# Kernel tuning notes

Measured on AMD Instinct MI355X. Metric: run time of the kernel, lower is better.

Reference implementation:

```python
import jax, jax.numpy as jnp
import numpy as np

B, N, U = 8, 2048, 256
BN_EPS = 1e-3  # keras BatchNormalization default epsilon
ADJ_DENSITY = 0.008  # ~16 neighbors per node on average


def setup_inputs() -> dict:
    key = jax.random.key(0)
    ks = jax.random.split(key, 16)
    s = 0.05  # weight scale ('random_normal' init is small-stddev in keras)
    x = jax.random.normal(ks[0], (B, N, U), jnp.float32)
    # sparse binary adjacency stored dense (per-sample SpMM pattern)
    adj = (jax.random.uniform(ks[1], (B, N, N)) < ADJ_DENSITY).astype(jnp.float32)
    nodal_mask = jnp.ones((B, N), jnp.float32)
    return {
        'x': x, 'adj': adj, 'nodal_mask': nodal_mask,
        'W_lin': jax.random.normal(ks[2], (U, U)) * s, 'b_lin': jnp.zeros((U,)),
        'Wq_mp': jax.random.normal(ks[3], (3, U, U)) * s, 'bq_mp': jnp.zeros((3, U)),
        'Wk_mp': jax.random.normal(ks[4], (3, U, U)) * s, 'bk_mp': jnp.zeros((3, U)),
        'Wv_mp': jax.random.normal(ks[5], (3, U, U)) * s, 'bv_mp': jnp.zeros((3, U)),
        'Wk_att': jax.random.normal(ks[6], (U, U)) * s,
        'Wv_att': jax.random.normal(ks[7], (U, U)) * s,
        'Wq_att': jax.random.normal(ks[8], (U, U)) * s,
        'Wo_att': jax.random.normal(ks[9], (U, U)) * s,
        'bn_gamma': jnp.ones((U,)), 'bn_beta': jnp.zeros((U,)),
        'bn_mean': jnp.zeros((U,)), 'bn_var': jnp.ones((U,)),
        'W_proj': jax.random.normal(ks[10], (U, U)) * s, 'b_proj': jnp.zeros((U,)),
        'W_res': jax.random.normal(ks[11], (U, U)) * s, 'b_res': jnp.zeros((U,)),
    }


def _dympn(x, adj, Ws, bs, mask):
    # 3 message-passing layers, each applied K_l=2 times (inference value)
    for i in range(3):
        for _ in range(2):
            xn = jnp.einsum('bmn,bnd->bmd', adj, x)  # batched SpMM (graph_conv mode)
            x = jax.nn.silu(jnp.einsum('bmd,de->bme', xn, Ws[i]) + bs[i])
    return x * mask[:, :, None]


def reference(x, adj, nodal_mask, W_lin, b_lin, Wq_mp, bq_mp, Wk_mp, bk_mp,
              Wv_mp, bv_mp, Wk_att, Wv_att, Wq_att, Wo_att,
              bn_gamma, bn_beta, bn_mean, bn_var, W_proj, b_proj, W_res, b_res):
    initial_x = x
    adj = jax.lax.stop_gradient(adj)
    h = jnp.einsum('bnd,de->bne', x, W_lin) + b_lin
    q = _dympn(h, adj, Wq_mp, bq_mp, nodal_mask)
    k = _dympn(h, adj, Wk_mp, bk_mp, nodal_mask)
    v = _dympn(h, adj, Wv_mp, bv_mp, nodal_mask)
    # linear attention
    m = nodal_mask[:, :, None]
    pk = jax.nn.silu(jnp.einsum('bnd,de->bne', k, Wk_att) * m)
    pv = jnp.einsum('bnd,de->bne', v, Wv_att) * m
    pq = jnp.einsum('bnd,de->bne', q, Wq_att)
    kv = jnp.einsum('bnd,bne->bde', pk, pv)       # [B,U,U]
    attn = jnp.einsum('bnd,bde->bne', pq, kv)
    attn = jnp.einsum('bnd,de->bne', attn, Wo_att)
    # batch norm (inference: moving stats) over last axis
    y = attn + initial_x
    y = bn_gamma * (y - bn_mean) * jax.lax.rsqrt(bn_var + BN_EPS) + bn_beta
    out = jax.nn.silu(jnp.einsum('bnd,de->bne', y, W_proj) + b_proj)
    out = out + jnp.einsum('bnd,de->bne', initial_x, W_res) + b_res
    out = out * nodal_mask[:, :, None]
    return out
```

## Files before the change

### kernel.cpp

```cpp
#include <hip/hip_runtime.h>
#include <stdint.h>

#define NB 8
#define NN 2048
#define NU 256
#define CAP 64
#define BNEPS 0.001f

typedef __attribute__((ext_vector_type(8))) short short8;
typedef __attribute__((ext_vector_type(4))) float floatx4;
typedef unsigned short u16;
typedef unsigned int u32;

__device__ __forceinline__ float bf2f(u16 u) {
  union { u32 i; float f; } c; c.i = ((u32)u) << 16; return c.f;
}
__device__ __forceinline__ u16 f2bf(float f) {
  union { float f; u32 i; } c; c.f = f;
  return (u16)((c.i + 0x7fffu + ((c.i >> 16) & 1u)) >> 16);
}
__device__ __forceinline__ void splitbf(float a, u16& h, u16& l) {
  h = f2bf(a);
  l = f2bf(a - bf2f(h));
}

enum : unsigned {
  F_BIAS = 2u, F_SILU = 4u, F_MASKPRE = 8u, F_MASKPOST = 16u,
  F_ADDX = 32u, F_BN = 64u, F_ADDT = 128u, F_BPERMAT = 512u,
  F_TPLANES = 1024u, F_OUTHL = 2048u
};

#define TP_MAT 524288
#define TP_LO  4194304
#define MSZ ((size_t)NN * NU)

struct WPtrs { const float* p[16]; };

__global__ __launch_bounds__(256) void prologue_k(
    WPtrs wp, u16* __restrict__ wdst,
    const float* __restrict__ x, u16* __restrict__ xdst, size_t xLo,
    const float* __restrict__ adj, int* __restrict__ cnt, int* __restrict__ idx)
{
  int bid = blockIdx.x;
  int tid = threadIdx.x;
  __shared__ int c0;
  if (bid < 512) {
    int gid = bid * 256 + tid;
    int mat = gid >> 13;
    int rem = gid & 8191;
    int kb = rem >> 10;
    int n = (rem >> 2) & 255;
    int slot = rem & 3;
    int qv = (slot - (n >> 1)) & 3;
    int k0 = kb * 32 + qv * 8;
    const float* W = wp.p[mat];
    u32 oh[4], ol[4];
#pragma unroll
    for (int t2 = 0; t2 < 4; t2++) {
      float f0 = W[(size_t)(k0 + 2 * t2) * 256 + n];
      float f1 = W[(size_t)(k0 + 2 * t2 + 1) * 256 + n];
      u16 h0, l0, h1, l1;
      splitbf(f0, h0, l0);
      splitbf(f1, h1, l1);
      oh[t2] = (u32)h0 | ((u32)h1 << 16);
      ol[t2] = (u32)l0 | ((u32)l1 << 16);
    }
    uint4 qh; qh.x = oh[0]; qh.y = oh[1]; qh.z = oh[2]; qh.w = oh[3];
    uint4 ql; ql.x = ol[0]; ql.y = ol[1]; ql.z = ol[2]; ql.w = ol[3];
    *(uint4*)(wdst + (size_t)gid * 8) = qh;
    *(uint4*)(wdst + 1048576 + (size_t)gid * 8) = ql;
  } else if (bid < 4608) {
    size_t i = ((size_t)(bid - 512) * 256 + tid) * 4;
    float4 v = *(const float4*)(x + i);
    u16 h0, l0, h1, l1, h2, l2, h3, l3;
    splitbf(v.x, h0, l0); splitbf(v.y, h1, l1);
    splitbf(v.z, h2, l2); splitbf(v.w, h3, l3);
    uint2 H; H.x = (u32)h0 | ((u32)h1 << 16); H.y = (u32)h2 | ((u32)h3 << 16);
    uint2 L; L.x = (u32)l0 | ((u32)l1 << 16); L.y = (u32)l2 | ((u32)l3 << 16);
    *(uint2*)(xdst + i) = H;
    *(uint2*)(xdst + xLo + i) = L;
  } else {
    int row = bid - 4608;
    const float* base = adj + (size_t)row * NN;
    if (tid == 0) c0 = 0;
    __syncthreads();
#pragma unroll
    for (int j = 0; j < 8; j++) {
      int n = j * 256 + tid;
      if (base[n] != 0.f) {
        int p = atomicAdd(&c0, 1);
        if (p < CAP) idx[(size_t)row * CAP + p] = n;
      }
    }
    __syncthreads();
    if (tid == 0) cnt[row] = (c0 < CAP ? c0 : CAP);
  }
}

template <unsigned F>
__device__ __forceinline__ void gemm_epi(
    floatx4 (&acc)[2][2], int b, int bm, int w, int m16, int q,
    const float* __restrict__ bias, const float* __restrict__ mask,
    const float* __restrict__ xf32,
    const float* __restrict__ gma, const float* __restrict__ bta,
    const float* __restrict__ bmu, const float* __restrict__ bvr,
    const float* __restrict__ addt, void* __restrict__ outp, size_t oLo)
{
#pragma unroll
  for (int mt = 0; mt < 2; mt++) {
    if (F & F_TPLANES) {
      u16* oh = (u16*)outp + (size_t)b * TP_MAT;
      u16* ol = oh + TP_LO;
      int gr0 = bm + mt * 16 + q * 4;
#pragma unroll
      for (int nt = 0; nt < 2; nt++) {
        int col = w * 32 + nt * 16 + m16;
        u16 hh[4], ll[4];
#pragma unroll
        for (int r = 0; r < 4; r++) {
          float t2 = acc[mt][nt][r];
          float mv = mask[b * NN + gr0 + r];
          if (F & F_MASKPRE) t2 *= mv;
          if (F & F_SILU) t2 = t2 / (1.f + __expf(-t2));
          if (F & F_MASKPOST) t2 *= mv;
          splitbf(t2, hh[r], ll[r]);
        }
        uint2 H2, L2v;
        H2.x = (u32)hh[0] | ((u32)hh[1] << 16);
        H2.y = (u32)hh[2] | ((u32)hh[3] << 16);
        L2v.x = (u32)ll[0] | ((u32)ll[1] << 16);
        L2v.y = (u32)ll[2] | ((u32)ll[3] << 16);
        *(uint2*)(oh + (size_t)col * 2048 + gr0) = H2;
        *(uint2*)(ol + (size_t)col * 2048 + gr0) = L2v;
      }
    } else {
#pragma unroll
      for (int r = 0; r < 4; r++) {
        int gr = bm + mt * 16 + q * 4 + r;
        float mval = 1.f;
        if (F & (F_MASKPRE | F_MASKPOST)) mval = mask[b * NN + gr];
#pragma unroll
        for (int nt = 0; nt < 2; nt++) {
          int col = w * 32 + nt * 16 + m16;
          float t2 = acc[mt][nt][r];
          if (F & F_BIAS) t2 += bias[col];
          if (F & F_MASKPRE) t2 *= mval;
          if (F & F_SILU) t2 = t2 / (1.f + __expf(-t2));
          if (F & F_ADDX) t2 += xf32[((size_t)b * NN + gr) * NU + col];
          if (F & F_BN) t2 = gma[col] * (t2 - bmu[col]) * rsqrtf(bvr[col] + BNEPS) + bta[col];
          if (F & F_ADDT) t2 += addt[((size_t)b * NN + gr) * NU + col];
          if (F & F_MASKPOST) t2 *= mval;
          size_t o = ((size_t)b * NN + gr) * NU + col;
          if (F & F_OUTHL) {
            u16 h0, l0;
            splitbf(t2, h0, l0);
            ((u16*)outp)[o] = h0;
            ((u16*)outp)[o + oLo] = l0;
          } else {
            ((float*)outp)[o] = t2;
          }
        }
      }
    }
  }
}

template <int NG, unsigned SF, unsigned F0, unsigned F1, unsigned F2, bool DK = false>
__global__ __launch_bounds__(512, 8) void gemm_k(
    const u16* __restrict__ A0, const u16* __restrict__ A1, const u16* __restrict__ A2,
    size_t aLo,
    const u16* __restrict__ W0, const u16* __restrict__ W1, const u16* __restrict__ W2,
    size_t wLo,
    const float* __restrict__ b0, const float* __restrict__ b1, const float* __restrict__ b2,
    const float* __restrict__ mask,
    const float* __restrict__ xf32,
    const float* __restrict__ gma, const float* __restrict__ bta,
    const float* __restrict__ bmu, const float* __restrict__ bvr,
    const float* __restrict__ addt,
    void* __restrict__ o0, void* __restrict__ o1, void* __restrict__ o2,
    size_t oLo,
    const float* __restrict__ gsrc,
    const float* __restrict__ sb0, const float* __restrict__ sb1, const float* __restrict__ sb2,
    const int* __restrict__ ncnt, const int* __restrict__ nidx)
{
  const int tid = threadIdx.x;
  const int id = blockIdx.x;
  const int xcd = id & 7;
  const int t = id >> 3;
  const int chain = (NG == 1) ? 0 : (t >> 6);
  const int xt = (NG == 1) ? t : (t & 63);
  const int b = xcd;
  const int bm = xt * 32;

  __shared__ alignas(16) u16 Ah[32 * 264];
  __shared__ alignas(16) u16 Al[32 * 264];

  const u16* Wsel = (chain == 0) ? W0 : (chain == 1 ? W1 : W2);
  if (F0 & F_BPERMAT) Wsel = W0 + (size_t)b * 65536;
  const u16* Whi = Wsel;
  const u16* Wlo = Whi + wLo;

  const int lane = tid & 63;
  const int w = tid >> 6;

  if constexpr (SF != 0u) {
    const float* __restrict__ gm = gsrc + ((size_t)chain * 8 + b) * MSZ;
    const float* sb = (chain == 0) ? sb0 : (chain == 1 ? sb1 : sb2);
    const int c = lane * 4;
    float4 bb = *(const float4*)(sb + c);
    const int r0 = w * 4;
    int cnts[4];
    const int* ips[4];
    float4 av[4];
    int rowids[4];
#pragma unroll
    for (int i = 0; i < 4; i++) {
      rowids[i] = b * NN + bm + r0 + i;
      cnts[i] = ncnt[rowids[i]];
      ips[i] = nidx + (size_t)rowids[i] * CAP;
      av[i].x = av[i].y = av[i].z = av[i].w = 0.f;
    }
    int maxc = cnts[0];
    maxc = cnts[1] > maxc ? cnts[1] : maxc;
    maxc = cnts[2] > maxc ? cnts[2] : maxc;
    maxc = cnts[3] > maxc ? cnts[3] : maxc;
    for (int e = 0; e + 4 <= maxc; e += 4) {
#pragma unroll
      for (int i = 0; i < 4; i++) {
        if (e + 4 <= cnts[i]) {
          int4 i4 = *(const int4*)(ips[i] + e);
          float4 v0 = *(const float4*)(gm + ((size_t)i4.x << 8) + c);
          float4 v1 = *(const float4*)(gm + ((size_t)i4.y << 8) + c);
          float4 v2 = *(const float4*)(gm + ((size_t)i4.z << 8) + c);
          float4 v3 = *(const float4*)(gm + ((size_t)i4.w << 8) + c);
          av[i].x += v0.x + v1.x + v2.x + v3.x;
          av[i].y += v0.y + v1.y + v2.y + v3.y;
          av[i].z += v0.z + v1.z + v2.z + v3.z;
          av[i].w += v0.w + v1.w + v2.w + v3.w;
        }
      }
    }
#pragma unroll
    for (int i = 0; i < 4; i++) {
      for (int e = cnts[i] & ~3; e < cnts[i]; e++) {
        float4 v = *(const float4*)(gm + ((size_t)ips[i][e] << 8) + c);
        av[i].x += v.x; av[i].y += v.y; av[i].z += v.z; av[i].w += v.w;
      }
    }
#pragma unroll
    for (int i = 0; i < 4; i++) {
      float ov[4] = {av[i].x + bb.x, av[i].y + bb.y, av[i].z + bb.z, av[i].w + bb.w};
      float mv = (SF & F_MASKPOST) ? mask[rowids[i]] : 1.f;
      u16 hh[4], ll[4];
#pragma unroll
      for (int j = 0; j < 4; j++) {
        float t2 = ov[j];
        if (SF & F_SILU) t2 = t2 / (1.f + __expf(-t2));
        if (SF & F_MASKPOST) t2 *= mv;
        splitbf(t2, hh[j], ll[j]);
      }
      uint2 H; H.x = (u32)hh[0] | ((u32)hh[1] << 16); H.y = (u32)hh[2] | ((u32)hh[3] << 16);
      uint2 L; L.x = (u32)ll[0] | ((u32)ll[1] << 16); L.y = (u32)ll[2] | ((u32)ll[3] << 16);
      *(uint2*)&Ah[(r0 + i) * 264 + c] = H;
      *(uint2*)&Al[(r0 + i) * 264 + c] = L;
    }
  } else {
    const u16* Abase = (chain == 0) ? A0 : (chain == 1 ? A1 : A2);
    const u16* Ahp = Abase + (size_t)b * MSZ;
    const u16* Alp = Ahp + aLo;
    {
      int s = tid;
      int r = s >> 4;
      int c = (s & 15) << 4;
      size_t ao = (size_t)(bm + r) * 256 + c;
      *(uint4*)&Ah[r * 264 + c] = *(const uint4*)(Ahp + ao);
      *(uint4*)&Ah[r * 264 + c + 8] = *(const uint4*)(Ahp + ao + 8);
      *(uint4*)&Al[r * 264 + c] = *(const uint4*)(Alp + ao);
      *(uint4*)&Al[r * 264 + c + 8] = *(const uint4*)(Alp + ao + 8);
    }
  }
  __syncthreads();

  const int m16 = lane & 15;
  const int q = lane >> 4;

  floatx4 acc[2][2];
#pragma unroll
  for (int i = 0; i < 2; i++)
#pragma unroll
    for (int j = 0; j < 2; j++) acc[i][j] = (floatx4){0.f, 0.f, 0.f, 0.f};

#pragma unroll
  for (int kk = 0; kk < 8; kk++) {
    short8 bh[2], bl2[2];
#pragma unroll
    for (int nt = 0; nt < 2; nt++) {
      int n = w * 32 + nt * 16 + m16;
      size_t off = (size_t)kk * 8192 + (size_t)n * 32 + (size_t)(((q + (n >> 1)) & 3) * 8);
      bh[nt] = *(const short8*)(Whi + off);
      bl2[nt] = *(const short8*)(Wlo + off);
    }
#pragma unroll
    for (int mt = 0; mt < 2; mt++) {
      int row = mt * 16 + m16;
      short8 ah = *(const short8*)&Ah[row * 264 + kk * 32 + q * 8];
      short8 al2 = *(const short8*)&Al[row * 264 + kk * 32 + q * 8];
#pragma unroll
      for (int nt = 0; nt < 2; nt++) {
        acc[mt][nt] = __builtin_amdgcn_mfma_f32_16x16x32_bf16(ah, bh[nt], acc[mt][nt], 0, 0, 0);
        acc[mt][nt] = __builtin_amdgcn_mfma_f32_16x16x32_bf16(al2, bh[nt], acc[mt][nt], 0, 0, 0);
        acc[mt][nt] = __builtin_amdgcn_mfma_f32_16x16x32_bf16(ah, bl2[nt], acc[mt][nt], 0, 0, 0);
      }
    }
  }

  if constexpr (DK) {
#pragma unroll
    for (int mt = 0; mt < 2; mt++)
#pragma unroll
      for (int nt = 0; nt < 2; nt++) {
        int col = w * 32 + nt * 16 + m16;
        float bp = b1[col];
#pragma unroll
        for (int r = 0; r < 4; r++) {
          float t2 = acc[mt][nt][r] + bp;
          acc[mt][nt][r] = t2 / (1.f + __expf(-t2));
        }
      }
    __syncthreads();
    {
      const u16* Ahp = A1 + (size_t)b * MSZ;
      const u16* Alp = Ahp + aLo;
      int s = tid;
      int r = s >> 4;
      int c = (s & 15) << 4;
      size_t ao = (size_t)(bm + r) * 256 + c;
      *(uint4*)&Ah[r * 264 + c] = *(const uint4*)(Ahp + ao);
      *(uint4*)&Ah[r * 264 + c + 8] = *(const uint4*)(Ahp + ao + 8);
      *(uint4*)&Al[r * 264 + c] = *(const uint4*)(Alp + ao);
      *(uint4*)&Al[r * 264 + c + 8] = *(const uint4*)(Alp + ao + 8);
    }
    __syncthreads();
    const u16* W1h = W1;
    const u16* W1l = W1 + wLo;
#pragma unroll
    for (int kk = 0; kk < 8; kk++) {
      short8 bh[2], bl2[2];
#pragma unroll
      for (int nt = 0; nt < 2; nt++) {
        int n = w * 32 + nt * 16 + m16;
        size_t off = (size_t)kk * 8192 + (size_t)n * 32 + (size_t)(((q + (n >> 1)) & 3) * 8);
        bh[nt] = *(const short8*)(W1h + off);
        bl2[nt] = *(const short8*)(W1l + off);
      }
#pragma unroll
      for (int mt = 0; mt < 2; mt++) {
        int row = mt * 16 + m16;
        short8 ah = *(const short8*)&Ah[row * 264 + kk * 32 + q * 8];
        short8 al2 = *(const short8*)&Al[row * 264 + kk * 32 + q * 8];
#pragma unroll
        for (int nt = 0; nt < 2; nt++) {
          acc[mt][nt] = __builtin_amdgcn_mfma_f32_16x16x32_bf16(ah, bh[nt], acc[mt][nt], 0, 0, 0);
          acc[mt][nt] = __builtin_amdgcn_mfma_f32_16x16x32_bf16(al2, bh[nt], acc[mt][nt], 0, 0, 0);
          acc[mt][nt] = __builtin_amdgcn_mfma_f32_16x16x32_bf16(ah, bl2[nt], acc[mt][nt], 0, 0, 0);
        }
      }
    }
  }

  if (NG == 1 || chain == 0)
    gemm_epi<F0>(acc, b, bm, w, m16, q, b0, mask, xf32, gma, bta, bmu, bvr, addt, o0, oLo);
  else if (chain == 1)
    gemm_epi<F1>(acc, b, bm, w, m16, q, b1, mask, xf32, gma, bta, bmu, bvr, addt, o1, oLo);
  else
    gemm_epi<F2>(acc, b, bm, w, m16, q, b2, mask, xf32, gma, bta, bmu, bvr, addt, o2, oLo);
}

__global__ __launch_bounds__(256, 2) void kv_k(
    const u16* __restrict__ pkT, const u16* __restrict__ pvT, float* __restrict__ part)
{
  int et = blockIdx.x * 128;
  int dt = blockIdx.y * 128;
  int z = blockIdx.z;
  int b = z & 7;
  int p = z >> 3;
  int tid = threadIdx.x;
  int lane = tid & 63, w = tid >> 6;
  int m16 = lane & 15, q = lane >> 4;

  const u16* pkh = pkT + (size_t)b * TP_MAT;
  const u16* pkl = pkh + TP_LO;
  const u16* pvh = pvT + (size_t)b * TP_MAT;
  const u16* pvl = pvh + TP_LO;

  int d_base = dt + (w >> 1) * 64 + m16;
  int e_base = et + (w & 1) * 64 + m16;

  floatx4 acc[4][4];
#pragma unroll
  for (int i = 0; i < 4; i++)
#pragma unroll
    for (int j = 0; j < 4; j++) acc[i][j] = (floatx4){0.f, 0.f, 0.f, 0.f};

#pragma unroll
  for (int kt = 0; kt < 8; kt++) {
    int kc = p * 256 + kt * 32 + q * 8;
    short8 ah[4], al[4], bh[4], bl[4];
#pragma unroll
    for (int mt = 0; mt < 4; mt++) {
      size_t o = (size_t)(d_base + mt * 16) * 2048 + kc;
      ah[mt] = *(const short8*)(pkh + o);
      al[mt] = *(const short8*)(pkl + o);
    }
#pragma unroll
    for (int nt = 0; nt < 4; nt++) {
      size_t o = (size_t)(e_base + nt * 16) * 2048 + kc;
      bh[nt] = *(const short8*)(pvh + o);
      bl[nt] = *(const short8*)(pvl + o);
    }
#pragma unroll
    for (int mt = 0; mt < 4; mt++)
#pragma unroll
      for (int nt = 0; nt < 4; nt++) {
        acc[mt][nt] = __builtin_amdgcn_mfma_f32_16x16x32_bf16(ah[mt], bh[nt], acc[mt][nt], 0, 0, 0);
        acc[mt][nt] = __builtin_amdgcn_mfma_f32_16x16x32_bf16(al[mt], bh[nt], acc[mt][nt], 0, 0, 0);
        acc[mt][nt] = __builtin_amdgcn_mfma_f32_16x16x32_bf16(ah[mt], bl[nt], acc[mt][nt], 0, 0, 0);
      }
  }

#pragma unroll
  for (int mt = 0; mt < 4; mt++)
#pragma unroll
    for (int r = 0; r < 4; r++) {
      int d = dt + (w >> 1) * 64 + mt * 16 + q * 4 + r;
#pragma unroll
      for (int nt = 0; nt < 4; nt++) {
        int e = et + (w & 1) * 64 + nt * 16 + m16;
        part[(size_t)z * 65536 + (size_t)d * 256 + e] = acc[mt][nt][r];
      }
    }
}

__global__ __launch_bounds__(256) void kv_conv_k(const float* __restrict__ part, u16* __restrict__ dst)
{
  int gid = blockIdx.x * 256 + threadIdx.x;
  int b = gid >> 13;
  int rem = gid & 8191;
  int kb = rem >> 10;
  int e = (rem >> 2) & 255;
  int slot = rem & 3;
  int qv = (slot - (e >> 1)) & 3;
  int d0 = kb * 32 + qv * 8;
  const float* src = part + (size_t)b * 65536 + (size_t)d0 * 256 + e;
  u32 oh[4], ol[4];
#pragma unroll
  for (int t2 = 0; t2 < 4; t2++) {
    float s0 = 0.f, s1 = 0.f;
#pragma unroll
    for (int pp = 0; pp < 8; pp++) {
      const float* sp = src + (size_t)pp * 524288 + t2 * 512;
      s0 += sp[0];
      s1 += sp[256];
    }
    u16 h0, l0, h1, l1;
    splitbf(s0, h0, l0);
    splitbf(s1, h1, l1);
    oh[t2] = (u32)h0 | ((u32)h1 << 16);
    ol[t2] = (u32)l0 | ((u32)l1 << 16);
  }
  uint4 qh; qh.x = oh[0]; qh.y = oh[1]; qh.z = oh[2]; qh.w = oh[3];
  uint4 ql; ql.x = ol[0]; ql.y = ol[1]; ql.z = ol[2]; ql.w = ol[3];
  *(uint4*)(dst + (size_t)gid * 8) = qh;
  *(uint4*)(dst + 524288 + (size_t)gid * 8) = ql;
}

extern "C" void kernel_launch(void* const* d_in, const int* in_sizes, int n_in,
                              void* d_out, int out_size, void* d_ws, size_t ws_size,
                              hipStream_t stream)
{
  const float* x = (const float*)d_in[0];
  const float* adj = (const float*)d_in[1];
  const float* mask = (const float*)d_in[2];
  const float* W_lin = (const float*)d_in[3];
  const float* b_lin = (const float*)d_in[4];
  const float* Wq_mp = (const float*)d_in[5];
  const float* bq_mp = (const float*)d_in[6];
  const float* Wk_mp = (const float*)d_in[7];
  const float* bk_mp = (const float*)d_in[8];
  const float* Wv_mp = (const float*)d_in[9];
  const float* bv_mp = (const float*)d_in[10];
  const float* Wk_att = (const float*)d_in[11];
  const float* Wv_att = (const float*)d_in[12];
  const float* Wq_att = (const float*)d_in[13];
  const float* Wo_att = (const float*)d_in[14];
  const float* bn_gamma = (const float*)d_in[15];
  const float* bn_beta = (const float*)d_in[16];
  const float* bn_mean = (const float*)d_in[17];
  const float* bn_var = (const float*)d_in[18];
  const float* W_proj = (const float*)d_in[19];
  const float* b_proj = (const float*)d_in[20];
  const float* W_res = (const float*)d_in[21];
  const float* b_res = (const float*)d_in[22];

  char* ws = (char*)d_ws;
  int* CNT    = (int*)(ws + 0);
  int* IDX    = (int*)(ws + (1ull << 20));
  u16* WSZ    = (u16*)(ws + (5ull << 20));
  u16* KVS    = (u16*)(ws + (9ull << 20));
  float* KVP  = (float*)(ws + (11ull << 20));
  u16* XHL    = (u16*)(ws + (27ull << 20));
  u16* HHL    = (u16*)(ws + (43ull << 20));
  float* GA   = (float*)(ws + (59ull << 20));
  float* GB   = (float*)(ws + (107ull << 20));
  u16* PKT    = (u16*)(ws + (155ull << 20));
  u16* PVT    = (u16*)(ws + (171ull << 20));
  u16* ATT    = (u16*)(ws + (187ull << 20));
  u16* YHL    = (u16*)(ws + (203ull << 20));

  const size_t WLO = 1048576;
  const size_t KLO = 524288;
  const size_t A8  = 8 * MSZ;

  u16* PQHL = HHL;

  WPtrs wp;
  wp.p[0] = W_lin;
  wp.p[1] = Wq_mp; wp.p[2] = Wq_mp + 65536; wp.p[3] = Wq_mp + 131072;
  wp.p[4] = Wk_mp; wp.p[5] = Wk_mp + 65536; wp.p[6] = Wk_mp + 131072;
  wp.p[7] = Wv_mp; wp.p[8] = Wv_mp + 65536; wp.p[9] = Wv_mp + 131072;
  wp.p[10] = Wk_att; wp.p[11] = Wv_att; wp.p[12] = Wq_att; wp.p[13] = Wo_att;
  wp.p[14] = W_proj; wp.p[15] = W_res;
  prologue_k<<<20992, 256, 0, stream>>>(wp, WSZ, x, XHL, A8, adj, CNT, IDX);

  gemm_k<1, 0u, F_BIAS | F_OUTHL, 0u, 0u><<<512, 512, 0, stream>>>(
      XHL, XHL, XHL, A8, WSZ, WSZ, WSZ, WLO,
      b_lin, nullptr, nullptr, mask, nullptr,
      bn_gamma, bn_beta, bn_mean, bn_var, nullptr,
      HHL, nullptr, nullptr, A8,
      nullptr, nullptr, nullptr, nullptr, CNT, IDX);

  gemm_k<3, 0u, 0u, 0u, 0u><<<1536, 512, 0, stream>>>(
      HHL, HHL, HHL, A8,
      WSZ + (size_t)1 * 65536, WSZ + (size_t)4 * 65536, WSZ + (size_t)7 * 65536, WLO,
      nullptr, nullptr, nullptr, mask, nullptr,
      bn_gamma, bn_beta, bn_mean, bn_var, nullptr,
      GA, GA + 8 * MSZ, GA + 16 * MSZ, 0,
      nullptr, nullptr, nullptr, nullptr, CNT, IDX);

  for (int s = 1; s < 6; s++) {
    int iw = s >> 1;
    int ib = (s - 1) >> 1;
    float* Gin = (s & 1) ? GA : GB;
    float* Gout = (s & 1) ? GB : GA;
    gemm_k<3, F_BIAS | F_SILU, 0u, 0u, 0u><<<1536, 512, 0, stream>>>(
        nullptr, nullptr, nullptr, 0,
        WSZ + (size_t)(1 + iw) * 65536, WSZ + (size_t)(4 + iw) * 65536,
        WSZ + (size_t)(7 + iw) * 65536, WLO,
        nullptr, nullptr, nullptr, mask, nullptr,
        bn_gamma, bn_beta, bn_mean, bn_var, nullptr,
        Gout, Gout + 8 * MSZ, Gout + 16 * MSZ, 0,
        Gin, bq_mp + ib * 256, bk_mp + ib * 256, bv_mp + ib * 256, CNT, IDX);
  }

  gemm_k<3, F_BIAS | F_SILU | F_MASKPOST,
         F_OUTHL, F_SILU | F_MASKPRE | F_TPLANES, F_MASKPOST | F_TPLANES>
      <<<1536, 512, 0, stream>>>(
      nullptr, nullptr, nullptr, 0,
      WSZ + (size_t)12 * 65536, WSZ + (size_t)10 * 65536, WSZ + (size_t)11 * 65536, WLO,
      nullptr, nullptr, nullptr, mask, nullptr,
      bn_gamma, bn_beta, bn_mean, bn_var, nullptr,
      PQHL, PKT, PVT, A8,
      GB, bq_mp + 512, bk_mp + 512, bv_mp + 512, CNT, IDX);

  kv_k<<<dim3(2, 2, 64), 256, 0, stream>>>(PKT, PVT, KVP);
  kv_conv_k<<<256, 256, 0, stream>>>(KVP, KVS);

  gemm_k<1, 0u, F_BPERMAT | F_OUTHL, 0u, 0u><<<512, 512, 0, stream>>>(
      PQHL, PQHL, PQHL, A8, KVS, KVS, KVS, KLO,
      nullptr, nullptr, nullptr, mask, nullptr,
      bn_gamma, bn_beta, bn_mean, bn_var, nullptr,
      ATT, nullptr, nullptr, A8,
      nullptr, nullptr, nullptr, nullptr, CNT, IDX);

  gemm_k<1, 0u, F_ADDX | F_BN | F_OUTHL, 0u, 0u><<<512, 512, 0, stream>>>(
      ATT, ATT, ATT, A8,
      WSZ + (size_t)13 * 65536, nullptr, nullptr, WLO,
      nullptr, nullptr, nullptr, mask, x,
      bn_gamma, bn_beta, bn_mean, bn_var, nullptr,
      YHL, nullptr, nullptr, A8,
      nullptr, nullptr, nullptr, nullptr, CNT, IDX);

  gemm_k<1, 0u, F_BIAS | F_MASKPOST, 0u, 0u, true><<<512, 512, 0, stream>>>(
      YHL, XHL, YHL, A8,
      WSZ + (size_t)14 * 65536, WSZ + (size_t)15 * 65536, nullptr, WLO,
      b_res, b_proj, nullptr, mask, nullptr,
      bn_gamma, bn_beta, bn_mean, bn_var, nullptr,
      d_out, nullptr, nullptr, 0,
      nullptr, nullptr, nullptr, nullptr, CNT, IDX);

  (void)in_sizes; (void)n_in; (void)out_size; (void)ws_size;
}
```

Before: 759.3 us.

## Pad SpMM gathers with zero row, branchless neighbor loop, nontemporal stores

Pads each neighbor index list to a multiple of four with -1 entries. Each per-batch G buffer gets a zeroed 256-float guard row in front, so index -1 reads zeros. This makes the SpMM gather loop branchless, with no remainder loop. Nontemporal stores are also added for the GEMM epilogue outputs and the kv partials, to reduce cache pollution from streaming writes. The costs are a changed workspace layout, extra prologue blocks to zero the guard rows, and some wasted gathers on padded entries.

```diff
diff --git a/kernel.cpp b/kernel.cpp
--- a/kernel.cpp
+++ b/kernel.cpp
@@ -6,11 +6,13 @@
 #define NU 256
 #define CAP 64
 #define BNEPS 0.001f
+#define GSTR ((size_t)(NN * NU + 256))
 
 typedef __attribute__((ext_vector_type(8))) short short8;
 typedef __attribute__((ext_vector_type(4))) float floatx4;
 typedef unsigned short u16;
 typedef unsigned int u32;
+typedef unsigned long long u64;
 
 __device__ __forceinline__ float bf2f(u16 u) {
   union { u32 i; float f; } c; c.i = ((u32)u) << 16; return c.f;
@@ -27,7 +29,7 @@
 enum : unsigned {
   F_BIAS = 2u, F_SILU = 4u, F_MASKPRE = 8u, F_MASKPOST = 16u,
   F_ADDX = 32u, F_BN = 64u, F_ADDT = 128u, F_BPERMAT = 512u,
-  F_TPLANES = 1024u, F_OUTHL = 2048u
+  F_TPLANES = 1024u, F_OUTHL = 2048u, F_NTOUT = 4096u, F_GSTRIDE = 8192u
 };
 
 #define TP_MAT 524288
@@ -39,7 +41,8 @@
 __global__ __launch_bounds__(256) void prologue_k(
     WPtrs wp, u16* __restrict__ wdst,
     const float* __restrict__ x, u16* __restrict__ xdst, size_t xLo,
-    const float* __restrict__ adj, int* __restrict__ cnt, int* __restrict__ idx)
+    const float* __restrict__ adj, int* __restrict__ cnt, int* __restrict__ idx,
+    float* __restrict__ ga, float* __restrict__ gb)
 {
   int bid = blockIdx.x;
   int tid = threadIdx.x;
@@ -79,7 +82,7 @@
     uint2 L; L.x = (u32)l0 | ((u32)l1 << 16); L.y = (u32)l2 | ((u32)l3 << 16);
     *(uint2*)(xdst + i) = H;
     *(uint2*)(xdst + xLo + i) = L;
-  } else {
+  } else if (bid < 20992) {
     int row = bid - 4608;
     const float* base = adj + (size_t)row * NN;
     if (tid == 0) c0 = 0;
@@ -93,7 +96,13 @@
       }
     }
     __syncthreads();
-    if (tid == 0) cnt[row] = (c0 < CAP ? c0 : CAP);
+    int cc = (c0 < CAP ? c0 : CAP);
+    for (int p = cc + tid; p < CAP; p += 256) idx[(size_t)row * CAP + p] = -1;
+    if (tid == 0) cnt[row] = cc;
+  } else {
+    int g = bid - 20992;
+    float* base = (g < 24 ? ga : gb) + (size_t)(g % 24) * GSTR;
+    base[tid] = 0.f;
   }
 }
 
@@ -130,8 +139,13 @@
         H2.y = (u32)hh[2] | ((u32)hh[3] << 16);
         L2v.x = (u32)ll[0] | ((u32)ll[1] << 16);
         L2v.y = (u32)ll[2] | ((u32)ll[3] << 16);
-        *(uint2*)(oh + (size_t)col * 2048 + gr0) = H2;
-        *(uint2*)(ol + (size_t)col * 2048 + gr0) = L2v;
+        if (F & F_NTOUT) {
+          __builtin_nontemporal_store(*(u64*)&H2, (u64*)(oh + (size_t)col * 2048 + gr0));
+          __builtin_nontemporal_store(*(u64*)&L2v, (u64*)(ol + (size_t)col * 2048 + gr0));
+        } else {
+          *(uint2*)(oh + (size_t)col * 2048 + gr0) = H2;
+          *(uint2*)(ol + (size_t)col * 2048 + gr0) = L2v;
+        }
       }
     } else {
 #pragma unroll
@@ -150,14 +164,22 @@
           if (F & F_BN) t2 = gma[col] * (t2 - bmu[col]) * rsqrtf(bvr[col] + BNEPS) + bta[col];
           if (F & F_ADDT) t2 += addt[((size_t)b * NN + gr) * NU + col];
           if (F & F_MASKPOST) t2 *= mval;
-          size_t o = ((size_t)b * NN + gr) * NU + col;
+          size_t o;
+          if (F & F_GSTRIDE) o = (size_t)b * GSTR + (size_t)gr * NU + col;
+          else o = ((size_t)b * NN + gr) * NU + col;
           if (F & F_OUTHL) {
             u16 h0, l0;
             splitbf(t2, h0, l0);
-            ((u16*)outp)[o] = h0;
-            ((u16*)outp)[o + oLo] = l0;
+            if (F & F_NTOUT) {
+              __builtin_nontemporal_store(h0, (u16*)outp + o);
+              __builtin_nontemporal_store(l0, (u16*)outp + o + oLo);
+            } else {
+              ((u16*)outp)[o] = h0;
+              ((u16*)outp)[o + oLo] = l0;
+            }
           } else {
-            ((float*)outp)[o] = t2;
+            if (F & F_NTOUT) __builtin_nontemporal_store(t2, (float*)outp + o);
+            else ((float*)outp)[o] = t2;
           }
         }
       }
@@ -204,47 +226,37 @@
   const int w = tid >> 6;
 
   if constexpr (SF != 0u) {
-    const float* __restrict__ gm = gsrc + ((size_t)chain * 8 + b) * MSZ;
+    const float* __restrict__ gm = gsrc + (size_t)(chain * 8 + b) * GSTR + 256;
     const float* sb = (chain == 0) ? sb0 : (chain == 1 ? sb1 : sb2);
     const int c = lane * 4;
     float4 bb = *(const float4*)(sb + c);
     const int r0 = w * 4;
-    int cnts[4];
     const int* ips[4];
     float4 av[4];
     int rowids[4];
+    int maxc = 0;
 #pragma unroll
     for (int i = 0; i < 4; i++) {
       rowids[i] = b * NN + bm + r0 + i;
-      cnts[i] = ncnt[rowids[i]];
+      int cn = ncnt[rowids[i]];
+      maxc = cn > maxc ? cn : maxc;
       ips[i] = nidx + (size_t)rowids[i] * CAP;
       av[i].x = av[i].y = av[i].z = av[i].w = 0.f;
     }
-    int maxc = cnts[0];
-    maxc = cnts[1] > maxc ? cnts[1] : maxc;
-    maxc = cnts[2] > maxc ? cnts[2] : maxc;
-    maxc = cnts[3] > maxc ? cnts[3] : maxc;
-    for (int e = 0; e + 4 <= maxc; e += 4) {
+    maxc = (maxc + 3) & ~3;
+#pragma unroll 1
+    for (int e = 0; e < maxc; e += 4) {
 #pragma unroll
       for (int i = 0; i < 4; i++) {
-        if (e + 4 <= cnts[i]) {
-          int4 i4 = *(const int4*)(ips[i] + e);
-          float4 v0 = *(const float4*)(gm + ((size_t)i4.x << 8) + c);
-          float4 v1 = *(const float4*)(gm + ((size_t)i4.y << 8) + c);
-          float4 v2 = *(const float4*)(gm + ((size_t)i4.z << 8) + c);
-          float4 v3 = *(const float4*)(gm + ((size_t)i4.w << 8) + c);
-          av[i].x += v0.x + v1.x + v2.x + v3.x;
-          av[i].y += v0.y + v1.y + v2.y + v3.y;
-          av[i].z += v0.z + v1.z + v2.z + v3.z;
-          av[i].w += v0.w + v1.w + v2.w + v3.w;
-        }
-      }
-    }
-#pragma unroll
-    for (int i = 0; i < 4; i++) {
-      for (int e = cnts[i] & ~3; e < cnts[i]; e++) {
-        float4 v = *(const float4*)(gm + ((size_t)ips[i][e] << 8) + c);
-        av[i].x += v.x; av[i].y += v.y; av[i].z += v.z; av[i].w += v.w;
+        int4 i4 = *(const int4*)(ips[i] + e);
+        float4 v0 = *(const float4*)(gm + (ptrdiff_t)i4.x * 256 + c);
+        float4 v1 = *(const float4*)(gm + (ptrdiff_t)i4.y * 256 + c);
+        float4 v2 = *(const float4*)(gm + (ptrdiff_t)i4.z * 256 + c);
+        float4 v3 = *(const float4*)(gm + (ptrdiff_t)i4.w * 256 + c);
+        av[i].x += v0.x + v1.x + v2.x + v3.x;
+        av[i].y += v0.y + v1.y + v2.y + v3.y;
+        av[i].z += v0.z + v1.z + v2.z + v3.z;
+        av[i].w += v0.w + v1.w + v2.w + v3.w;
       }
     }
 #pragma unroll
@@ -436,7 +448,8 @@
 #pragma unroll
       for (int nt = 0; nt < 4; nt++) {
         int e = et + (w & 1) * 64 + nt * 16 + m16;
-        part[(size_t)z * 65536 + (size_t)d * 256 + e] = acc[mt][nt][r];
+        __builtin_nontemporal_store(acc[mt][nt][r],
+                                    &part[(size_t)z * 65536 + (size_t)d * 256 + e]);
       }
     }
 }
@@ -511,15 +524,16 @@
   u16* XHL    = (u16*)(ws + (27ull << 20));
   u16* HHL    = (u16*)(ws + (43ull << 20));
   float* GA   = (float*)(ws + (59ull << 20));
-  float* GB   = (float*)(ws + (107ull << 20));
-  u16* PKT    = (u16*)(ws + (155ull << 20));
-  u16* PVT    = (u16*)(ws + (171ull << 20));
-  u16* ATT    = (u16*)(ws + (187ull << 20));
-  u16* YHL    = (u16*)(ws + (203ull << 20));
+  float* GB   = (float*)(ws + (110ull << 20));
+  u16* PKT    = (u16*)(ws + (161ull << 20));
+  u16* PVT    = (u16*)(ws + (177ull << 20));
+  u16* ATT    = (u16*)(ws + (193ull << 20));
+  u16* YHL    = (u16*)(ws + (209ull << 20));
 
   const size_t WLO = 1048576;
   const size_t KLO = 524288;
   const size_t A8  = 8 * MSZ;
+  const unsigned FG = F_NTOUT | F_GSTRIDE;
 
   u16* PQHL = HHL;
 
@@ -530,7 +544,7 @@
   wp.p[7] = Wv_mp; wp.p[8] = Wv_mp + 65536; wp.p[9] = Wv_mp + 131072;
   wp.p[10] = Wk_att; wp.p[11] = Wv_att; wp.p[12] = Wq_att; wp.p[13] = Wo_att;
   wp.p[14] = W_proj; wp.p[15] = W_res;
-  prologue_k<<<20992, 256, 0, stream>>>(wp, WSZ, x, XHL, A8, adj, CNT, IDX);
+  prologue_k<<<21040, 256, 0, stream>>>(wp, WSZ, x, XHL, A8, adj, CNT, IDX, GA, GB);
 
   gemm_k<1, 0u, F_BIAS | F_OUTHL, 0u, 0u><<<512, 512, 0, stream>>>(
       XHL, XHL, XHL, A8, WSZ, WSZ, WSZ, WLO,
@@ -539,12 +553,12 @@
       HHL, nullptr, nullptr, A8,
       nullptr, nullptr, nullptr, nullptr, CNT, IDX);
 
-  gemm_k<3, 0u, 0u, 0u, 0u><<<1536, 512, 0, stream>>>(
+  gemm_k<3, 0u, FG, FG, FG><<<1536, 512, 0, stream>>>(
       HHL, HHL, HHL, A8,
       WSZ + (size_t)1 * 65536, WSZ + (size_t)4 * 65536, WSZ + (size_t)7 * 65536, WLO,
       nullptr, nullptr, nullptr, mask, nullptr,
       bn_gamma, bn_beta, bn_mean, bn_var, nullptr,
-      GA, GA + 8 * MSZ, GA + 16 * MSZ, 0,
+      GA + 256, GA + 8 * GSTR + 256, GA + 16 * GSTR + 256, 0,
       nullptr, nullptr, nullptr, nullptr, CNT, IDX);
 
   for (int s = 1; s < 6; s++) {
@@ -552,18 +566,19 @@
     int ib = (s - 1) >> 1;
     float* Gin = (s & 1) ? GA : GB;
     float* Gout = (s & 1) ? GB : GA;
-    gemm_k<3, F_BIAS | F_SILU, 0u, 0u, 0u><<<1536, 512, 0, stream>>>(
+    gemm_k<3, F_BIAS | F_SILU, FG, FG, FG><<<1536, 512, 0, stream>>>(
         nullptr, nullptr, nullptr, 0,
         WSZ + (size_t)(1 + iw) * 65536, WSZ + (size_t)(4 + iw) * 65536,
         WSZ + (size_t)(7 + iw) * 65536, WLO,
         nullptr, nullptr, nullptr, mask, nullptr,
         bn_gamma, bn_beta, bn_mean, bn_var, nullptr,
-        Gout, Gout + 8 * MSZ, Gout + 16 * MSZ, 0,
+        Gout + 256, Gout + 8 * GSTR + 256, Gout + 16 * GSTR + 256, 0,
         Gin, bq_mp + ib * 256, bk_mp + ib * 256, bv_mp + ib * 256, CNT, IDX);
   }
 
   gemm_k<3, F_BIAS | F_SILU | F_MASKPOST,
-         F_OUTHL, F_SILU | F_MASKPRE | F_TPLANES, F_MASKPOST | F_TPLANES>
+         F_OUTHL | F_NTOUT, F_SILU | F_MASKPRE | F_TPLANES | F_NTOUT,
+         F_MASKPOST | F_TPLANES | F_NTOUT>
       <<<1536, 512, 0, stream>>>(
       nullptr, nullptr, nullptr, 0,
       WSZ + (size_t)12 * 65536, WSZ + (size_t)10 * 65536, WSZ + (size_t)11 * 65536, WLO,
```

Measured after the change: 883.5 us. +16.4%, slower.

## Split fused three-chain message-passing launches into per-chain sequential launches

Applied to the files above, without the earlier changes.

Replaces the 3-wide fused gemm_k launches (1536 blocks covering q, k and v chains together) with a separate 512-block launch sequence for each chain. The final per-chain projection launches are split out the same way. PQHL gets its own workspace buffer instead of aliasing HHL, because HHL is still read by later chains. The likely aim is better cache locality, since each chain's working set (its adjacency gathers and weights) stays resident in L2/LLC across its steps. The cost is three times as many launches, and each launch has fewer blocks to fill the GPU.

```diff
diff --git a/kernel.cpp b/kernel.cpp
--- a/kernel.cpp
+++ b/kernel.cpp
@@ -516,12 +516,11 @@
   u16* PVT    = (u16*)(ws + (171ull << 20));
   u16* ATT    = (u16*)(ws + (187ull << 20));
   u16* YHL    = (u16*)(ws + (203ull << 20));
+  u16* PQHL   = (u16*)(ws + (219ull << 20));
 
   const size_t WLO = 1048576;
   const size_t KLO = 524288;
   const size_t A8  = 8 * MSZ;
-
-  u16* PQHL = HHL;
 
   WPtrs wp;
   wp.p[0] = W_lin;
@@ -539,38 +538,59 @@
       HHL, nullptr, nullptr, A8,
       nullptr, nullptr, nullptr, nullptr, CNT, IDX);
 
-  gemm_k<3, 0u, 0u, 0u, 0u><<<1536, 512, 0, stream>>>(
-      HHL, HHL, HHL, A8,
-      WSZ + (size_t)1 * 65536, WSZ + (size_t)4 * 65536, WSZ + (size_t)7 * 65536, WLO,
-      nullptr, nullptr, nullptr, mask, nullptr,
-      bn_gamma, bn_beta, bn_mean, bn_var, nullptr,
-      GA, GA + 8 * MSZ, GA + 16 * MSZ, 0,
-      nullptr, nullptr, nullptr, nullptr, CNT, IDX);
-
-  for (int s = 1; s < 6; s++) {
-    int iw = s >> 1;
-    int ib = (s - 1) >> 1;
-    float* Gin = (s & 1) ? GA : GB;
-    float* Gout = (s & 1) ? GB : GA;
-    gemm_k<3, F_BIAS | F_SILU, 0u, 0u, 0u><<<1536, 512, 0, stream>>>(
-        nullptr, nullptr, nullptr, 0,
-        WSZ + (size_t)(1 + iw) * 65536, WSZ + (size_t)(4 + iw) * 65536,
-        WSZ + (size_t)(7 + iw) * 65536, WLO,
+  const float* mpb[3] = {bq_mp, bk_mp, bv_mp};
+  for (int c = 0; c < 3; c++) {
+    const u16* Wc = WSZ + (size_t)(1 + 3 * c) * 65536;
+    float* Gc[2] = {GA + (size_t)c * 8 * MSZ, GB + (size_t)c * 8 * MSZ};
+
+    gemm_k<1, 0u, 0u, 0u, 0u><<<512, 512, 0, stream>>>(
+        HHL, HHL, HHL, A8, Wc, Wc, Wc, WLO,
         nullptr, nullptr, nullptr, mask, nullptr,
         bn_gamma, bn_beta, bn_mean, bn_var, nullptr,
-        Gout, Gout + 8 * MSZ, Gout + 16 * MSZ, 0,
-        Gin, bq_mp + ib * 256, bk_mp + ib * 256, bv_mp + ib * 256, CNT, IDX);
-  }
-
-  gemm_k<3, F_BIAS | F_SILU | F_MASKPOST,
-         F_OUTHL, F_SILU | F_MASKPRE | F_TPLANES, F_MASKPOST | F_TPLANES>
-      <<<1536, 512, 0, stream>>>(
-      nullptr, nullptr, nullptr, 0,
-      WSZ + (size_t)12 * 65536, WSZ + (size_t)10 * 65536, WSZ + (size_t)11 * 65536, WLO,
-      nullptr, nullptr, nullptr, mask, nullptr,
-      bn_gamma, bn_beta, bn_mean, bn_var, nullptr,
-      PQHL, PKT, PVT, A8,
-      GB, bq_mp + 512, bk_mp + 512, bv_mp + 512, CNT, IDX);
+        Gc[0], nullptr, nullptr, 0,
+        nullptr, nullptr, nullptr, nullptr, CNT, IDX);
+
+    for (int s = 1; s < 6; s++) {
+      int iw = s >> 1;
+      int ib = (s - 1) >> 1;
+      float* Gin = Gc[(s + 1) & 1];
+      float* Gout = Gc[s & 1];
+      gemm_k<1, F_BIAS | F_SILU, 0u, 0u, 0u><<<512, 512, 0, stream>>>(
+          nullptr, nullptr, nullptr, 0,
+          Wc + (size_t)iw * 65536, Wc, Wc, WLO,
+          nullptr, nullptr, nullptr, mask, nullptr,
+          bn_gamma, bn_beta, bn_mean, bn_var, nullptr,
+          Gout, nullptr, nullptr, 0,
+          Gin, mpb[c] + ib * 256, nullptr, nullptr, CNT, IDX);
+    }
+
+    if (c == 0)
+      gemm_k<1, F_BIAS | F_SILU | F_MASKPOST, F_OUTHL, 0u, 0u><<<512, 512, 0, stream>>>(
+          nullptr, nullptr, nullptr, 0,
+          WSZ + (size_t)12 * 65536, nullptr, nullptr, WLO,
+          nullptr, nullptr, nullptr, mask, nullptr,
+          bn_gamma, bn_beta, bn_mean, bn_var, nullptr,
+          PQHL, nullptr, nullptr, A8,
+          Gc[1], mpb[c] + 512, nullptr, nullptr, CNT, IDX);
+    else if (c == 1)
+      gemm_k<1, F_BIAS | F_SILU | F_MASKPOST, F_SILU | F_MASKPRE | F_TPLANES, 0u, 0u>
+          <<<512, 512, 0, stream>>>(
+          nullptr, nullptr, nullptr, 0,
+          WSZ + (size_t)10 * 65536, nullptr, nullptr, WLO,
+          nullptr, nullptr, nullptr, mask, nullptr,
+          bn_gamma, bn_beta, bn_mean, bn_var, nullptr,
+          PKT, nullptr, nullptr, A8,
+          Gc[1], mpb[c] + 512, nullptr, nullptr, CNT, IDX);
+    else
+      gemm_k<1, F_BIAS | F_SILU | F_MASKPOST, F_MASKPOST | F_TPLANES, 0u, 0u>
+          <<<512, 512, 0, stream>>>(
+          nullptr, nullptr, nullptr, 0,
+          WSZ + (size_t)11 * 65536, nullptr, nullptr, WLO,
+          nullptr, nullptr, nullptr, mask, nullptr,
+          bn_gamma, bn_beta, bn_mean, bn_var, nullptr,
+          PVT, nullptr, nullptr, A8,
+          Gc[1], mpb[c] + 512, nullptr, nullptr, CNT, IDX);
+  }
 
   kv_k<<<dim3(2, 2, 64), 256, 0, stream>>>(PKT, PVT, KVP);
   kv_conv_k<<<256, 256, 0, stream>>>(KVP, KVS);
```

Result: slower. 828.5 us (+9.1%).
